# Kernel optimization log

Measured on AMD Instinct MI355X. Metric: run time of the kernel, lower is better.

The kernel has to match this reference:

```python
import jax, jax.numpy as jnp
import numpy as np


def _norm_cdf(x):
    # standard normal CDF via erf
    return 0.5 * (1.0 + jax.lax.erf(x * np.float32(1.0 / np.sqrt(2.0))))


def setup_inputs() -> dict:
    key = jax.random.key(0)
    k1, k2 = jax.random.split(key)
    shape = (8192, 4096)
    y_pred = jax.random.normal(k1, shape, dtype=jnp.float32)
    y_true = jax.random.normal(k2, shape, dtype=jnp.float32)
    sigma_v, sigma_u = 1.0, 0.5
    log_std_v = jnp.asarray(np.log(sigma_v), dtype=jnp.float32)
    log_std_u = jnp.asarray(np.log(sigma_u), dtype=jnp.float32)
    return {"y_pred": y_pred, "y_true": y_true,
            "log_std_v": log_std_v, "log_std_u": log_std_u}


def reference(y_pred, y_true, log_std_v, log_std_u):
    std_v = jnp.exp(log_std_v)
    std_u = jnp.exp(log_std_u)
    sigma2 = std_v ** 2 + std_u ** 2
    sigma = jnp.sqrt(sigma2)
    llamda = jnp.sqrt(std_u ** 2 / std_v ** 2)
    resid = y_true - y_pred
    # torch code detaches before the CDF (numpy round-trip) -> stop_gradient
    cdf_arg = jax.lax.stop_gradient(-llamda * resid / sigma)
    ff = _norm_cdf(cdf_arg)
    log_likelihood = (-0.5 * jnp.log(jnp.float32(np.pi / 2.0))
                      - 0.5 * jnp.log(sigma2)
                      + jnp.log(ff)
                      - resid ** 2 / (2.0 * sigma2))
    return -jnp.mean(log_likelihood)
```

## Files before the change

### kernel.cpp

```cpp
#include <hip/hip_runtime.h>
#include <math.h>


__device__ __forceinline__ float fast_log_ncdf_erfarg(float x) {
    float ax = fabsf(x);
    float t  = __builtin_amdgcn_rcpf(fmaf(0.3275911f, ax, 1.0f));
    float p  = fmaf(t, 1.061405429f, -1.453152027f);
    p = fmaf(t, p, 1.421413741f);
    p = fmaf(t, p, -0.284496736f);
    p = fmaf(t, p, 0.254829592f);
    p *= t;
    float e  = __expf(-ax * ax);
    float ea = fmaf(-p, e, 1.0f);
    float ev = copysignf(ea, x);
    return __logf(fmaf(0.5f, ev, 0.5f));
}

__global__ __launch_bounds__(256) void gnll_kernel(
    const float4* __restrict__ yp, const float4* __restrict__ yt,
    const float* __restrict__ lsv, const float* __restrict__ lsu,
    float* __restrict__ out, int n4, float neg_inv_n)
{
    const float std_v  = __expf(lsv[0]);
    const float std_u  = __expf(lsu[0]);
    const float sigma2 = std_v * std_v + std_u * std_u;
    const float sigma  = sqrtf(sigma2);
    const float llamda = std_u / std_v;
    const float karg   = -llamda / sigma * 0.70710678118654752f;
    const float c0     = -0.5f * logf(1.57079632679489662f)
                         - 0.5f * logf(sigma2);
    const float inv2s2 = 0.5f / sigma2;

    float acc = 0.0f;
    int   cnt = 0;
    int idx    = blockIdx.x * blockDim.x + threadIdx.x;
    int stride = gridDim.x * blockDim.x;

    for (int i = idx; i < n4; i += stride) {
        float4 p = yp[i];
        float4 t = yt[i];
        float r0 = t.x - p.x;
        float r1 = t.y - p.y;
        float r2 = t.z - p.z;
        float r3 = t.w - p.w;
        float ll0 = fast_log_ncdf_erfarg(karg * r0) - r0 * r0 * inv2s2;
        float ll1 = fast_log_ncdf_erfarg(karg * r1) - r1 * r1 * inv2s2;
        float ll2 = fast_log_ncdf_erfarg(karg * r2) - r2 * r2 * inv2s2;
        float ll3 = fast_log_ncdf_erfarg(karg * r3) - r3 * r3 * inv2s2;
        acc += (ll0 + ll1) + (ll2 + ll3);
        cnt += 4;
    }
    acc = fmaf((float)cnt, c0, acc);

    #pragma unroll
    for (int off = 32; off > 0; off >>= 1)
        acc += __shfl_down(acc, off, 64);

    __shared__ float ws[4];
    int lane = threadIdx.x & 63;
    int wid  = threadIdx.x >> 6;
    if (lane == 0) ws[wid] = acc;
    __syncthreads();
    if (threadIdx.x == 0) {
        float s = (ws[0] + ws[1]) + (ws[2] + ws[3]);
        atomicAdd(out, s * neg_inv_n);
    }
}

extern "C" void kernel_launch(void* const* d_in, const int* in_sizes, int n_in,
                              void* d_out, int out_size, void* d_ws, size_t ws_size,
                              hipStream_t stream) {
    const float4* yp = (const float4*)d_in[0];
    const float4* yt = (const float4*)d_in[1];
    const float* lsv = (const float*)d_in[2];
    const float* lsu = (const float*)d_in[3];
    float* out = (float*)d_out;

    long long n = (long long)in_sizes[0];
    int n4 = (int)(n / 4);
    float neg_inv_n = -1.0f / (float)n;

    hipMemsetAsync(d_out, 0, sizeof(float), stream);

    int block = 256;
    int grid  = 2048;
    gnll_kernel<<<grid, block, 0, stream>>>(yp, yt, lsv, lsu, out, n4, neg_inv_n);
}
```

Before: 63.98 us.

## Double-buffer grid-stride loads in register groups and reuse r^2 in exp

Restructures the grid-stride loop into groups of four float4 loads per input, ping-ponging between two register sets. Loads for the next group are issued before computing the current one, so more memory requests are in flight per thread. The exp argument now reuses the squared residual scaled by a precomputed constant, which saves a multiply per element. The cost is higher register pressure, plus a scalar tail loop for the remainder.

```diff
diff --git a/kernel.cpp b/kernel.cpp
--- a/kernel.cpp
+++ b/kernel.cpp
@@ -2,7 +2,9 @@
 #include <math.h>
 
 
-__device__ __forceinline__ float fast_log_ncdf_erfarg(float x) {
+__device__ __forceinline__ float ll_elem(float r, float karg, float nk2, float inv2s2) {
+    float r2 = r * r;
+    float x  = karg * r;
     float ax = fabsf(x);
     float t  = __builtin_amdgcn_rcpf(fmaf(0.3275911f, ax, 1.0f));
     float p  = fmaf(t, 1.061405429f, -1.453152027f);
@@ -10,10 +12,10 @@
     p = fmaf(t, p, -0.284496736f);
     p = fmaf(t, p, 0.254829592f);
     p *= t;
-    float e  = __expf(-ax * ax);
+    float e  = __expf(nk2 * r2);
     float ea = fmaf(-p, e, 1.0f);
     float ev = copysignf(ea, x);
-    return __logf(fmaf(0.5f, ev, 0.5f));
+    return __logf(fmaf(0.5f, ev, 0.5f)) - r2 * inv2s2;
 }
 
 __global__ __launch_bounds__(256) void gnll_kernel(
@@ -27,29 +29,61 @@
     const float sigma  = sqrtf(sigma2);
     const float llamda = std_u / std_v;
     const float karg   = -llamda / sigma * 0.70710678118654752f;
+    const float nk2    = -karg * karg;
     const float c0     = -0.5f * logf(1.57079632679489662f)
                          - 0.5f * logf(sigma2);
     const float inv2s2 = 0.5f / sigma2;
 
     float acc = 0.0f;
     int   cnt = 0;
-    int idx    = blockIdx.x * blockDim.x + threadIdx.x;
-    int stride = gridDim.x * blockDim.x;
+    const int tid = blockIdx.x * blockDim.x + threadIdx.x;
+    const int nth = gridDim.x * blockDim.x;
 
-    for (int i = idx; i < n4; i += stride) {
+    float4 pA0, pA1, pA2, pA3, tA0, tA1, tA2, tA3;
+    float4 pB0, pB1, pB2, pB3, tB0, tB1, tB2, tB3;
+
+#define LOAD_A(g) { int b_ = (g) * nth * 4 + tid;                                   \
+    pA0 = yp[b_]; pA1 = yp[b_ + nth]; pA2 = yp[b_ + 2*nth]; pA3 = yp[b_ + 3*nth];   \
+    tA0 = yt[b_]; tA1 = yt[b_ + nth]; tA2 = yt[b_ + 2*nth]; tA3 = yt[b_ + 3*nth]; }
+#define LOAD_B(g) { int b_ = (g) * nth * 4 + tid;                                   \
+    pB0 = yp[b_]; pB1 = yp[b_ + nth]; pB2 = yp[b_ + 2*nth]; pB3 = yp[b_ + 3*nth];   \
+    tB0 = yt[b_]; tB1 = yt[b_ + nth]; tB2 = yt[b_ + 2*nth]; tB3 = yt[b_ + 3*nth]; }
+#define COMP1(P, T) { float s_ =                                                    \
+      ll_elem(T.x - P.x, karg, nk2, inv2s2) + ll_elem(T.y - P.y, karg, nk2, inv2s2) \
+    + ll_elem(T.z - P.z, karg, nk2, inv2s2) + ll_elem(T.w - P.w, karg, nk2, inv2s2);\
+    acc += s_; }
+#define COMP_A { COMP1(pA0, tA0) COMP1(pA1, tA1) COMP1(pA2, tA2) COMP1(pA3, tA3) cnt += 16; }
+#define COMP_B { COMP1(pB0, tB0) COMP1(pB1, tB1) COMP1(pB2, tB2) COMP1(pB3, tB3) cnt += 16; }
+
+    const int ngroups = n4 / (nth * 4);
+    if (ngroups > 0) {
+        LOAD_A(0)
+        int g = 0;
+        for (; g + 2 < ngroups; g += 2) {
+            LOAD_B(g + 1)
+            COMP_A
+            LOAD_A(g + 2)
+            COMP_B
+        }
+        if (g + 1 < ngroups) {
+            LOAD_B(g + 1)
+            COMP_A
+            COMP_B
+        } else {
+            COMP_A
+        }
+    }
+
+    for (int i = ngroups * nth * 4 + tid; i < n4; i += nth) {
         float4 p = yp[i];
         float4 t = yt[i];
-        float r0 = t.x - p.x;
-        float r1 = t.y - p.y;
-        float r2 = t.z - p.z;
-        float r3 = t.w - p.w;
-        float ll0 = fast_log_ncdf_erfarg(karg * r0) - r0 * r0 * inv2s2;
-        float ll1 = fast_log_ncdf_erfarg(karg * r1) - r1 * r1 * inv2s2;
-        float ll2 = fast_log_ncdf_erfarg(karg * r2) - r2 * r2 * inv2s2;
-        float ll3 = fast_log_ncdf_erfarg(karg * r3) - r3 * r3 * inv2s2;
-        acc += (ll0 + ll1) + (ll2 + ll3);
+        acc += ll_elem(t.x - p.x, karg, nk2, inv2s2)
+             + ll_elem(t.y - p.y, karg, nk2, inv2s2)
+             + ll_elem(t.z - p.z, karg, nk2, inv2s2)
+             + ll_elem(t.w - p.w, karg, nk2, inv2s2);
         cnt += 4;
     }
+
     acc = fmaf((float)cnt, c0, acc);
 
     #pragma unroll
```

After: 58.03 us. 9.3% less time.

## Issue four float4 loads per thread up front with larger grid

Applied to the files above, without the earlier changes.

Restructures the grid-stride loop so that, when possible, each thread loads four float4 pairs at once before computing. This increases memory-level parallelism. The grid is enlarged so that each thread handles exactly four vectors, and a fallback loop covers the ragged case. The erf exponent is also computed from the precomputed -karg^2 times r^2. The larger grid adds more block-level atomics to the output.

```diff
diff --git a/kernel.cpp b/kernel.cpp
--- a/kernel.cpp
+++ b/kernel.cpp
@@ -2,7 +2,9 @@
 #include <math.h>
 
 
-__device__ __forceinline__ float fast_log_ncdf_erfarg(float x) {
+__device__ __forceinline__ float ll_elem(float r, float karg, float nk2, float inv2s2) {
+    float r2 = r * r;
+    float x  = karg * r;
     float ax = fabsf(x);
     float t  = __builtin_amdgcn_rcpf(fmaf(0.3275911f, ax, 1.0f));
     float p  = fmaf(t, 1.061405429f, -1.453152027f);
@@ -10,10 +12,10 @@
     p = fmaf(t, p, -0.284496736f);
     p = fmaf(t, p, 0.254829592f);
     p *= t;
-    float e  = __expf(-ax * ax);
+    float e  = __expf(nk2 * r2);
     float ea = fmaf(-p, e, 1.0f);
     float ev = copysignf(ea, x);
-    return __logf(fmaf(0.5f, ev, 0.5f));
+    return __logf(fmaf(0.5f, ev, 0.5f)) - r2 * inv2s2;
 }
 
 __global__ __launch_bounds__(256) void gnll_kernel(
@@ -27,30 +29,61 @@
     const float sigma  = sqrtf(sigma2);
     const float llamda = std_u / std_v;
     const float karg   = -llamda / sigma * 0.70710678118654752f;
+    const float nk2    = -karg * karg;
     const float c0     = -0.5f * logf(1.57079632679489662f)
                          - 0.5f * logf(sigma2);
     const float inv2s2 = 0.5f / sigma2;
 
+    const int tid = blockIdx.x * blockDim.x + threadIdx.x;
+    const int nth = gridDim.x * blockDim.x;
+
     float acc = 0.0f;
-    int   cnt = 0;
-    int idx    = blockIdx.x * blockDim.x + threadIdx.x;
-    int stride = gridDim.x * blockDim.x;
 
-    for (int i = idx; i < n4; i += stride) {
-        float4 p = yp[i];
-        float4 t = yt[i];
-        float r0 = t.x - p.x;
-        float r1 = t.y - p.y;
-        float r2 = t.z - p.z;
-        float r3 = t.w - p.w;
-        float ll0 = fast_log_ncdf_erfarg(karg * r0) - r0 * r0 * inv2s2;
-        float ll1 = fast_log_ncdf_erfarg(karg * r1) - r1 * r1 * inv2s2;
-        float ll2 = fast_log_ncdf_erfarg(karg * r2) - r2 * r2 * inv2s2;
-        float ll3 = fast_log_ncdf_erfarg(karg * r3) - r3 * r3 * inv2s2;
-        acc += (ll0 + ll1) + (ll2 + ll3);
-        cnt += 4;
+    const int i0 = tid;
+    const int i1 = tid + nth;
+    const int i2 = tid + 2 * nth;
+    const int i3 = tid + 3 * nth;
+
+    if (i3 < n4) {
+        float4 p0 = yp[i0];
+        float4 t0 = yt[i0];
+        float4 p1 = yp[i1];
+        float4 t1 = yt[i1];
+        float4 p2 = yp[i2];
+        float4 t2 = yt[i2];
+        float4 p3 = yp[i3];
+        float4 t3 = yt[i3];
+
+        float s0 = ll_elem(t0.x - p0.x, karg, nk2, inv2s2)
+                 + ll_elem(t0.y - p0.y, karg, nk2, inv2s2)
+                 + ll_elem(t0.z - p0.z, karg, nk2, inv2s2)
+                 + ll_elem(t0.w - p0.w, karg, nk2, inv2s2);
+        float s1 = ll_elem(t1.x - p1.x, karg, nk2, inv2s2)
+                 + ll_elem(t1.y - p1.y, karg, nk2, inv2s2)
+                 + ll_elem(t1.z - p1.z, karg, nk2, inv2s2)
+                 + ll_elem(t1.w - p1.w, karg, nk2, inv2s2);
+        float s2 = ll_elem(t2.x - p2.x, karg, nk2, inv2s2)
+                 + ll_elem(t2.y - p2.y, karg, nk2, inv2s2)
+                 + ll_elem(t2.z - p2.z, karg, nk2, inv2s2)
+                 + ll_elem(t2.w - p2.w, karg, nk2, inv2s2);
+        float s3 = ll_elem(t3.x - p3.x, karg, nk2, inv2s2)
+                 + ll_elem(t3.y - p3.y, karg, nk2, inv2s2)
+                 + ll_elem(t3.z - p3.z, karg, nk2, inv2s2)
+                 + ll_elem(t3.w - p3.w, karg, nk2, inv2s2);
+        acc = (s0 + s1) + (s2 + s3) + 16.0f * c0;
+    } else {
+        int cnt = 0;
+        for (int i = i0; i < n4; i += nth) {
+            float4 p = yp[i];
+            float4 t = yt[i];
+            acc += ll_elem(t.x - p.x, karg, nk2, inv2s2)
+                 + ll_elem(t.y - p.y, karg, nk2, inv2s2)
+                 + ll_elem(t.z - p.z, karg, nk2, inv2s2)
+                 + ll_elem(t.w - p.w, karg, nk2, inv2s2);
+            cnt += 4;
+        }
+        acc = fmaf((float)cnt, c0, acc);
     }
-    acc = fmaf((float)cnt, c0, acc);
 
     #pragma unroll
     for (int off = 32; off > 0; off >>= 1)
@@ -83,6 +116,6 @@
     hipMemsetAsync(d_out, 0, sizeof(float), stream);
 
     int block = 256;
-    int grid  = 2048;
+    int grid  = 8192;
     gnll_kernel<<<grid, block, 0, stream>>>(yp, yt, lsv, lsu, out, n4, neg_inv_n);
 }
```

Result: slower. 121.7 us (+90.2%).
